# Performance work log

Measured on AMD Instinct MI355X. Metric: run time of the kernel, lower is better.

The kernel has to match this reference:

```python
import jax, jax.numpy as jnp
import numpy as np

RES = 1024
NUM_ROOMS = 8
N_AGENTS = 5_000_000


def setup_inputs() -> dict:
    key = jax.random.key(0)
    k1, k2, k3 = jax.random.split(key, 3)
    agent_positions = jax.random.uniform(k1, (N_AGENTS, 2), dtype=jnp.float32)
    room_params = jax.random.uniform(k2, (NUM_ROOMS, 4), dtype=jnp.float32)
    # torch init: params[:, 2:] = params[:, 2:] * 0.1 + 0.05  (room sigmas)
    room_params = room_params.at[:, 2:].set(room_params[:, 2:] * 0.1 + 0.05)
    wall_density = jax.random.uniform(k3, (RES, RES), dtype=jnp.float32)
    return {
        "agent_positions": agent_positions,
        "room_params": room_params,
        "wall_density": wall_density,
    }


def reference(agent_positions, room_params, wall_density):
    res = wall_density.shape[0]
    lin = jnp.linspace(0.0, 1.0, res, dtype=wall_density.dtype)
    x_grid, y_grid = jnp.meshgrid(lin, lin, indexing="ij")  # [res,res]

    # Per-room Gaussian density maps, vectorized over rooms -> [R,res,res]
    cx = room_params[:, 0, None, None]
    cy = room_params[:, 1, None, None]
    sx = room_params[:, 2, None, None]
    sy = room_params[:, 3, None, None]
    spatial_layout = jnp.exp(
        -((x_grid - cx) ** 2 / (2.0 * sx**2) + (y_grid - cy) ** 2 / (2.0 * sy**2))
    )

    # Agent flow histogram via single fused scatter-add
    ix = jnp.clip((agent_positions[:, 0] * res).astype(jnp.int32), 0, res - 1)
    iy = jnp.clip((agent_positions[:, 1] * res).astype(jnp.int32), 0, res - 1)
    flow_field = jnp.zeros((res, res), dtype=wall_density.dtype).at[ix, iy].add(1.0)
    flow_field = flow_field / (flow_field.max() + 1e-6)

    dynamic_layout = spatial_layout * (1.0 - wall_density[None, :, :])
    return (dynamic_layout, flow_field)
```

## Files before the change

kernel.cpp:

```cpp
#include <hip/hip_runtime.h>

#define RES 1024
#define NROOMS 8
#define NBUCKETS 256
#define BINS_PER_BUCKET (4 * RES)
#define CAP 32768
#define SWPB 8
#define NBLK 512
#define F4PT 10
#define STG_MAX (512 * F4PT * 2)

typedef unsigned int u32x4 __attribute__((ext_vector_type(4)));
typedef float        f32x4 __attribute__((ext_vector_type(4)));

__device__ __forceinline__ void dyn_cell(
    const float* __restrict__ room_params,
    const float4* __restrict__ wall,
    float4* __restrict__ dyn, int idx)
{
    int i  = idx >> 8;
    int j0 = (idx & 255) << 2;
    const float inv1023 = 1.0f / 1023.0f;
    float x  = (float)i * inv1023;
    float y0 = (float)(j0 + 0) * inv1023;
    float y1 = (float)(j0 + 1) * inv1023;
    float y2 = (float)(j0 + 2) * inv1023;
    float y3 = (float)(j0 + 3) * inv1023;

    float4 w = wall[idx];
    float omx = 1.0f - w.x;
    float omy = 1.0f - w.y;
    float omz = 1.0f - w.z;
    float omw = 1.0f - w.w;

    const int plane4 = (RES * RES) / 4;
    #pragma unroll
    for (int r = 0; r < NROOMS; ++r) {
        float cx = room_params[4 * r + 0];
        float cy = room_params[4 * r + 1];
        float sx = room_params[4 * r + 2];
        float sy = room_params[4 * r + 3];
        float isx = 1.0f / (2.0f * sx * sx);
        float isy = 1.0f / (2.0f * sy * sy);
        float dx = x - cx;
        float ax = dx * dx * isx;
        float d0 = y0 - cy, d1 = y1 - cy, d2 = y2 - cy, d3 = y3 - cy;
        f32x4 d;
        d.x = __expf(-(ax + d0 * d0 * isy)) * omx;
        d.y = __expf(-(ax + d1 * d1 * isy)) * omy;
        d.z = __expf(-(ax + d2 * d2 * isy)) * omz;
        d.w = __expf(-(ax + d3 * d3 * isy)) * omw;
        __builtin_nontemporal_store(
            d, reinterpret_cast<f32x4*>(&dyn[(size_t)r * plane4 + idx]));
    }
}

__global__ __launch_bounds__(512, 4) void scatter_kernel(
    const float4* __restrict__ pos, int n4, int nagents,
    unsigned short* __restrict__ buf, unsigned int* __restrict__ cursor,
    const float* __restrict__ room_params,
    const float4* __restrict__ wall,
    float4* __restrict__ dyn)
{
    __shared__ unsigned int   cnt[SWPB][NBUCKETS];
    __shared__ unsigned int   pstart[NBUCKETS];
    __shared__ unsigned int   ptotal[NBUCKETS];
    __shared__ unsigned int   gbase[NBUCKETS];
    __shared__ unsigned int   wsum[4];
    __shared__ unsigned short staged[STG_MAX];
    __shared__ unsigned int   codeLDS[2 * F4PT][512];

    int tid  = threadIdx.x;
    int wv   = tid >> 6;
    int lane = tid & 63;

    #pragma unroll
    for (int i = 0; i < (SWPB * NBUCKETS) / 512; ++i)
        ((unsigned int*)cnt)[tid + 512 * i] = 0u;
    __syncthreads();

    int chunk = (n4 + NBLK - 1) / NBLK;
    int start = blockIdx.x * chunk;
    int end   = min(start + chunk, n4);

    #pragma unroll
    for (int k = 0; k < F4PT; ++k) {
        int i4 = start + (k << 9) + tid;
        if (i4 < end) {
            float4 p = pos[i4];
            int ix0 = min(max((int)(p.x * 1024.0f), 0), 1023);
            int iy0 = min(max((int)(p.y * 1024.0f), 0), 1023);
            int ix1 = min(max((int)(p.z * 1024.0f), 0), 1023);
            int iy1 = min(max((int)(p.w * 1024.0f), 0), 1023);
            unsigned int b0 = (unsigned int)(ix0 >> 2);
            unsigned int b1 = (unsigned int)(ix1 >> 2);
            unsigned int bin0 = (unsigned int)(((ix0 & 3) << 10) | iy0);
            unsigned int bin1 = (unsigned int)(((ix1 & 3) << 10) | iy1);
            unsigned int r0 = atomicAdd(&cnt[wv][b0], 1u);
            unsigned int r1 = atomicAdd(&cnt[wv][b1], 1u);
            codeLDS[2 * k][tid]     = (b0 << 23) | (r0 << 12) | bin0;
            codeLDS[2 * k + 1][tid] = (b1 << 23) | (r1 << 12) | bin1;
        } else {
            codeLDS[2 * k][tid]     = 0xFFFFFFFFu;
            codeLDS[2 * k + 1][tid] = 0xFFFFFFFFu;
        }
    }

    dyn_cell(room_params, wall, dyn, blockIdx.x * 512 + tid);

    __syncthreads();

    if (tid < NBUCKETS) {
        unsigned int run = 0;
        #pragma unroll
        for (int w = 0; w < SWPB; ++w) {
            unsigned int c = cnt[w][tid];
            cnt[w][tid] = run;
            run += c;
        }
        ptotal[tid] = run;
        gbase[tid]  = run ? atomicAdd(&cursor[tid], run) : 0u;
        unsigned int t = run;
        #pragma unroll
        for (int off = 1; off < 64; off <<= 1) {
            unsigned int v = (unsigned int)__shfl_up((int)t, off, 64);
            if (lane >= off) t += v;
        }
        if (lane == 63) wsum[wv] = t;
        pstart[tid] = t - run;
    }
    __syncthreads();
    if (tid < NBUCKETS) {
        unsigned int off = 0;
        #pragma unroll
        for (int w = 0; w < 3; ++w) if (w < wv) off += wsum[w];
        unsigned int ps = pstart[tid] + off;
        pstart[tid] = ps;
        #pragma unroll
        for (int w = 0; w < SWPB; ++w) cnt[w][tid] += ps;
    }
    __syncthreads();

    #pragma unroll
    for (int k = 0; k < 2 * F4PT; ++k) {
        unsigned int u = codeLDS[k][tid];
        if (u != 0xFFFFFFFFu) {
            unsigned int b   = u >> 23;
            unsigned int r   = (u >> 12) & 0x7FFu;
            unsigned int bin = u & 0xFFFu;
            staged[cnt[wv][b] + r] = (unsigned short)bin;
        }
    }
    __syncthreads();

    #pragma unroll 4
    for (int bb = 0; bb < 32; ++bb) {
        int b = (wv << 5) + bb;
        unsigned int n  = ptotal[b];
        unsigned int ps = pstart[b];
        unsigned int gb = gbase[b];
        for (unsigned int e = lane; e < n; e += 64) {
            unsigned int p = gb + e;
            if (p < CAP) buf[b * CAP + p] = staged[ps + e];
        }
    }

    if (blockIdx.x == 0 && tid == 0 && (nagents & 1)) {
        const float* t = (const float*)pos;
        float px = t[2 * (nagents - 1)];
        float py = t[2 * (nagents - 1) + 1];
        int ix = min(max((int)(px * 1024.0f), 0), 1023);
        int iy = min(max((int)(py * 1024.0f), 0), 1023);
        unsigned int b = (unsigned int)(ix >> 2);
        unsigned int p = atomicAdd(&cursor[b], 1u);
        if (p < CAP) buf[b * CAP + p] = (unsigned short)(((ix & 3) << 10) | iy);
    }
}

__global__ __launch_bounds__(1024) void hist_build_kernel(
    const unsigned short* __restrict__ buf,
    const unsigned int* __restrict__ cursor,
    unsigned int* __restrict__ counts,
    unsigned int* __restrict__ out_max)
{
    __shared__ __align__(16) unsigned int h[BINS_PER_BUCKET];
    int b = blockIdx.x, tid = threadIdx.x;
    #pragma unroll
    for (int i = 0; i < BINS_PER_BUCKET / 1024; ++i) h[tid + 1024 * i] = 0u;
    __syncthreads();

    unsigned int n = min(cursor[b], (unsigned int)CAP);
    const unsigned short* seg = buf + (size_t)b * CAP;
    unsigned int n2 = n & ~1u;
    for (unsigned int i = 2 * tid; i < n2; i += 2048) {
        unsigned int u = *(const unsigned int*)(seg + i);
        atomicAdd(&h[u & 0xFFFFu], 1u);
        atomicAdd(&h[u >> 16], 1u);
    }
    if (tid == 0 && (n & 1)) atomicAdd(&h[seg[n - 1]], 1u);
    __syncthreads();

    u32x4 v = ((const u32x4*)h)[tid];
    ((u32x4*)counts)[(size_t)b * (BINS_PER_BUCKET / 4) + tid] = v;
    unsigned int m = max(max(v.x, v.y), max(v.z, v.w));
    #pragma unroll
    for (int off = 32; off > 0; off >>= 1)
        m = max(m, (unsigned int)__shfl_down((int)m, off, 64));
    __shared__ unsigned int sm[16];
    if ((tid & 63) == 0) sm[tid >> 6] = m;
    __syncthreads();
    if (tid == 0) {
        #pragma unroll
        for (int w = 1; w < 16; ++w) m = max(m, sm[w]);
        atomicMax(out_max, m);
    }
}

__global__ __launch_bounds__(256) void norm_kernel(
    float* __restrict__ flow, const unsigned int* __restrict__ maxp)
{
    int idx = blockIdx.x * blockDim.x + threadIdx.x;
    uint4 c = ((const uint4*)flow)[idx];
    float inv = 1.0f / ((float)(*maxp) + 1e-6f);
    ((float4*)flow)[idx] = make_float4((float)c.x * inv, (float)c.y * inv,
                                       (float)c.z * inv, (float)c.w * inv);
}

__global__ __launch_bounds__(256) void hist_atomic_kernel(
    const float4* __restrict__ pos, int n4, int nagents,
    unsigned int* __restrict__ counts)
{
    int idx = blockIdx.x * blockDim.x + threadIdx.x;
    int stride = gridDim.x * blockDim.x;
    for (int i = idx; i < n4; i += stride) {
        float4 p = pos[i];
        int ix0 = min(max((int)(p.x * 1024.0f), 0), 1023);
        int iy0 = min(max((int)(p.y * 1024.0f), 0), 1023);
        int ix1 = min(max((int)(p.z * 1024.0f), 0), 1023);
        int iy1 = min(max((int)(p.w * 1024.0f), 0), 1023);
        atomicAdd(&counts[(ix0 << 10) + iy0], 1u);
        atomicAdd(&counts[(ix1 << 10) + iy1], 1u);
    }
    if (idx == 0 && (nagents & 1)) {
        const float* t = (const float*)pos;
        int ix = min(max((int)(t[2 * (nagents - 1)] * 1024.0f), 0), 1023);
        int iy = min(max((int)(t[2 * (nagents - 1) + 1] * 1024.0f), 0), 1023);
        atomicAdd(&counts[(ix << 10) + iy], 1u);
    }
}

__global__ __launch_bounds__(256) void max_kernel(
    const uint4* __restrict__ counts, unsigned int* __restrict__ out_max)
{
    int idx = blockIdx.x * blockDim.x + threadIdx.x;
    int stride = gridDim.x * blockDim.x;
    unsigned int m = 0;
    const int n4 = (RES * RES) / 4;
    for (int i = idx; i < n4; i += stride) {
        uint4 c = counts[i];
        m = max(m, max(max(c.x, c.y), max(c.z, c.w)));
    }
    #pragma unroll
    for (int off = 32; off > 0; off >>= 1)
        m = max(m, (unsigned int)__shfl_down((int)m, off, 64));
    __shared__ unsigned int sm[4];
    if ((threadIdx.x & 63) == 0) sm[threadIdx.x >> 6] = m;
    __syncthreads();
    if (threadIdx.x == 0) {
        m = max(max(sm[0], sm[1]), max(sm[2], sm[3]));
        atomicMax(out_max, m);
    }
}

__global__ __launch_bounds__(256) void final_full_kernel(
    const float* __restrict__ room_params,
    const float4* __restrict__ wall,
    float4* __restrict__ dyn,
    float* __restrict__ flow,
    const unsigned int* __restrict__ maxp)
{
    int idx = blockIdx.x * blockDim.x + threadIdx.x;
    uint4 c = ((const uint4*)flow)[idx];
    float inv = 1.0f / ((float)(*maxp) + 1e-6f);
    ((float4*)flow)[idx] = make_float4((float)c.x * inv, (float)c.y * inv,
                                       (float)c.z * inv, (float)c.w * inv);
    dyn_cell(room_params, wall, dyn, idx);
}

extern "C" void kernel_launch(void* const* d_in, const int* in_sizes, int n_in,
                              void* d_out, int out_size, void* d_ws, size_t ws_size,
                              hipStream_t stream) {
    const float* agents      = (const float*)d_in[0];
    const float* room_params = (const float*)d_in[1];
    const float* wall        = (const float*)d_in[2];

    float* dyn  = (float*)d_out;
    float* flow = (float*)d_out + (size_t)NROOMS * RES * RES;
    unsigned int* counts = (unsigned int*)flow;

    int nagents = in_sizes[0] / 2;
    int n4 = nagents / 2;

    size_t need = 2048 + (size_t)NBUCKETS * CAP * sizeof(unsigned short);

    bool fits = ((n4 + NBLK - 1) / NBLK) <= (F4PT * 512);

    if (ws_size >= need && fits) {
        unsigned int*   cursor = (unsigned int*)d_ws;
        unsigned int*   maxp   = (unsigned int*)((char*)d_ws + 1024);
        unsigned short* buf    = (unsigned short*)((char*)d_ws + 2048);

        (void)hipMemsetAsync(d_ws, 0, 2048, stream);
        scatter_kernel<<<NBLK, 512, 0, stream>>>(
            (const float4*)agents, n4, nagents, buf, cursor,
            room_params, (const float4*)wall, (float4*)dyn);
        hist_build_kernel<<<NBUCKETS, 1024, 0, stream>>>(buf, cursor, counts, maxp);
        norm_kernel<<<(RES * RES / 4) / 256, 256, 0, stream>>>(flow, maxp);
    } else {
        unsigned int* maxp = (unsigned int*)d_ws;
        (void)hipMemsetAsync(flow, 0, (size_t)RES * RES * sizeof(float), stream);
        (void)hipMemsetAsync(maxp, 0, sizeof(unsigned int), stream);
        hist_atomic_kernel<<<1280, 256, 0, stream>>>((const float4*)agents, n4, nagents, counts);
        max_kernel<<<256, 256, 0, stream>>>((const uint4*)counts, maxp);
        final_full_kernel<<<(RES * RES / 4) / 256, 256, 0, stream>>>(
            room_params, (const float4*)wall, (float4*)dyn, flow, maxp);
    }
}
```

Before: 118.4 us.

## Fuse normalization into histogram kernel via grid barrier, move dyn work, two-pass scatter

The dynamic-layout computation moves from the scatter kernel into the histogram kernel. The separate normalization kernel is removed: the histogram kernel counts finished blocks with an atomic, spins until all 256 have published their max, then writes normalized floats directly. The scatter kernel now reads positions twice (a count pass, then a placement pass) instead of holding codes in LDS. It also uses 1024 smaller blocks with higher occupancy. This drops one kernel launch and the count round trip through memory, at the cost of re-reading the input and relying on all 256 blocks being co-resident for the spin barrier.

Result: slower. 139.1 us (+17.5%).

```diff
diff --git a/kernel.cpp b/kernel.cpp
--- a/kernel.cpp
+++ b/kernel.cpp
@@ -6,8 +6,8 @@
 #define BINS_PER_BUCKET (4 * RES)
 #define CAP 32768
 #define SWPB 8
-#define NBLK 512
-#define F4PT 10
+#define NBLK 1024
+#define F4PT 5
 #define STG_MAX (512 * F4PT * 2)
 
 typedef unsigned int u32x4 __attribute__((ext_vector_type(4)));
@@ -55,12 +55,9 @@
     }
 }
 
-__global__ __launch_bounds__(512, 4) void scatter_kernel(
+__global__ __launch_bounds__(512, 8) void scatter_kernel(
     const float4* __restrict__ pos, int n4, int nagents,
-    unsigned short* __restrict__ buf, unsigned int* __restrict__ cursor,
-    const float* __restrict__ room_params,
-    const float4* __restrict__ wall,
-    float4* __restrict__ dyn)
+    unsigned short* __restrict__ buf, unsigned int* __restrict__ cursor)
 {
     __shared__ unsigned int   cnt[SWPB][NBUCKETS];
     __shared__ unsigned int   pstart[NBUCKETS];
@@ -68,7 +65,6 @@
     __shared__ unsigned int   gbase[NBUCKETS];
     __shared__ unsigned int   wsum[4];
     __shared__ unsigned short staged[STG_MAX];
-    __shared__ unsigned int   codeLDS[2 * F4PT][512];
 
     int tid  = threadIdx.x;
     int wv   = tid >> 6;
@@ -82,6 +78,50 @@
     int chunk = (n4 + NBLK - 1) / NBLK;
     int start = blockIdx.x * chunk;
     int end   = min(start + chunk, n4);
+
+    #pragma unroll
+    for (int k = 0; k < F4PT; ++k) {
+        int i4 = start + (k << 9) + tid;
+        if (i4 < end) {
+            float4 p = pos[i4];
+            int ix0 = min(max((int)(p.x * 1024.0f), 0), 1023);
+            int ix1 = min(max((int)(p.z * 1024.0f), 0), 1023);
+            atomicAdd(&cnt[wv][ix0 >> 2], 1u);
+            atomicAdd(&cnt[wv][ix1 >> 2], 1u);
+        }
+    }
+    __syncthreads();
+
+    if (tid < NBUCKETS) {
+        unsigned int run = 0;
+        #pragma unroll
+        for (int w = 0; w < SWPB; ++w) {
+            unsigned int c = cnt[w][tid];
+            cnt[w][tid] = run;
+            run += c;
+        }
+        ptotal[tid] = run;
+        gbase[tid]  = run ? atomicAdd(&cursor[tid], run) : 0u;
+        unsigned int t = run;
+        #pragma unroll
+        for (int off = 1; off < 64; off <<= 1) {
+            unsigned int v = (unsigned int)__shfl_up((int)t, off, 64);
+            if (lane >= off) t += v;
+        }
+        if (lane == 63) wsum[wv] = t;
+        pstart[tid] = t - run;
+    }
+    __syncthreads();
+    if (tid < NBUCKETS) {
+        unsigned int off = 0;
+        #pragma unroll
+        for (int w = 0; w < 3; ++w) if (w < wv) off += wsum[w];
+        unsigned int ps = pstart[tid] + off;
+        pstart[tid] = ps;
+        #pragma unroll
+        for (int w = 0; w < SWPB; ++w) cnt[w][tid] += ps;
+    }
+    __syncthreads();
 
     #pragma unroll
     for (int k = 0; k < F4PT; ++k) {
@@ -92,63 +132,10 @@
             int iy0 = min(max((int)(p.y * 1024.0f), 0), 1023);
             int ix1 = min(max((int)(p.z * 1024.0f), 0), 1023);
             int iy1 = min(max((int)(p.w * 1024.0f), 0), 1023);
-            unsigned int b0 = (unsigned int)(ix0 >> 2);
-            unsigned int b1 = (unsigned int)(ix1 >> 2);
-            unsigned int bin0 = (unsigned int)(((ix0 & 3) << 10) | iy0);
-            unsigned int bin1 = (unsigned int)(((ix1 & 3) << 10) | iy1);
-            unsigned int r0 = atomicAdd(&cnt[wv][b0], 1u);
-            unsigned int r1 = atomicAdd(&cnt[wv][b1], 1u);
-            codeLDS[2 * k][tid]     = (b0 << 23) | (r0 << 12) | bin0;
-            codeLDS[2 * k + 1][tid] = (b1 << 23) | (r1 << 12) | bin1;
-        } else {
-            codeLDS[2 * k][tid]     = 0xFFFFFFFFu;
-            codeLDS[2 * k + 1][tid] = 0xFFFFFFFFu;
-        }
-    }
-
-    dyn_cell(room_params, wall, dyn, blockIdx.x * 512 + tid);
-
-    __syncthreads();
-
-    if (tid < NBUCKETS) {
-        unsigned int run = 0;
-        #pragma unroll
-        for (int w = 0; w < SWPB; ++w) {
-            unsigned int c = cnt[w][tid];
-            cnt[w][tid] = run;
-            run += c;
-        }
-        ptotal[tid] = run;
-        gbase[tid]  = run ? atomicAdd(&cursor[tid], run) : 0u;
-        unsigned int t = run;
-        #pragma unroll
-        for (int off = 1; off < 64; off <<= 1) {
-            unsigned int v = (unsigned int)__shfl_up((int)t, off, 64);
-            if (lane >= off) t += v;
-        }
-        if (lane == 63) wsum[wv] = t;
-        pstart[tid] = t - run;
-    }
-    __syncthreads();
-    if (tid < NBUCKETS) {
-        unsigned int off = 0;
-        #pragma unroll
-        for (int w = 0; w < 3; ++w) if (w < wv) off += wsum[w];
-        unsigned int ps = pstart[tid] + off;
-        pstart[tid] = ps;
-        #pragma unroll
-        for (int w = 0; w < SWPB; ++w) cnt[w][tid] += ps;
-    }
-    __syncthreads();
-
-    #pragma unroll
-    for (int k = 0; k < 2 * F4PT; ++k) {
-        unsigned int u = codeLDS[k][tid];
-        if (u != 0xFFFFFFFFu) {
-            unsigned int b   = u >> 23;
-            unsigned int r   = (u >> 12) & 0x7FFu;
-            unsigned int bin = u & 0xFFFu;
-            staged[cnt[wv][b] + r] = (unsigned short)bin;
+            unsigned int s0 = atomicAdd(&cnt[wv][ix0 >> 2], 1u);
+            staged[s0] = (unsigned short)(((ix0 & 3) << 10) | iy0);
+            unsigned int s1 = atomicAdd(&cnt[wv][ix1 >> 2], 1u);
+            staged[s1] = (unsigned short)(((ix1 & 3) << 10) | iy1);
         }
     }
     __syncthreads();
@@ -177,13 +164,19 @@
     }
 }
 
-__global__ __launch_bounds__(1024) void hist_build_kernel(
+__global__ __launch_bounds__(1024) void hist_dyn_kernel(
     const unsigned short* __restrict__ buf,
     const unsigned int* __restrict__ cursor,
-    unsigned int* __restrict__ counts,
-    unsigned int* __restrict__ out_max)
+    const float* __restrict__ room_params,
+    const float4* __restrict__ wall,
+    float4* __restrict__ dyn,
+    float* __restrict__ flow,
+    unsigned int* __restrict__ maxp,
+    unsigned int* __restrict__ done)
 {
     __shared__ __align__(16) unsigned int h[BINS_PER_BUCKET];
+    __shared__ unsigned int sm[16];
+    __shared__ float sinv;
     int b = blockIdx.x, tid = threadIdx.x;
     #pragma unroll
     for (int i = 0; i < BINS_PER_BUCKET / 1024; ++i) h[tid + 1024 * i] = 0u;
@@ -201,29 +194,39 @@
     __syncthreads();
 
     u32x4 v = ((const u32x4*)h)[tid];
-    ((u32x4*)counts)[(size_t)b * (BINS_PER_BUCKET / 4) + tid] = v;
     unsigned int m = max(max(v.x, v.y), max(v.z, v.w));
     #pragma unroll
     for (int off = 32; off > 0; off >>= 1)
         m = max(m, (unsigned int)__shfl_down((int)m, off, 64));
-    __shared__ unsigned int sm[16];
     if ((tid & 63) == 0) sm[tid >> 6] = m;
     __syncthreads();
     if (tid == 0) {
         #pragma unroll
         for (int w = 1; w < 16; ++w) m = max(m, sm[w]);
-        atomicMax(out_max, m);
-    }
-}
-
-__global__ __launch_bounds__(256) void norm_kernel(
-    float* __restrict__ flow, const unsigned int* __restrict__ maxp)
-{
-    int idx = blockIdx.x * blockDim.x + threadIdx.x;
-    uint4 c = ((const uint4*)flow)[idx];
-    float inv = 1.0f / ((float)(*maxp) + 1e-6f);
-    ((float4*)flow)[idx] = make_float4((float)c.x * inv, (float)c.y * inv,
-                                       (float)c.z * inv, (float)c.w * inv);
+        atomicMax(maxp, m);
+        __hip_atomic_fetch_add(done, 1u, __ATOMIC_RELEASE,
+                               __HIP_MEMORY_SCOPE_AGENT);
+    }
+
+    dyn_cell(room_params, wall, dyn, b * 1024 + tid);
+
+    if (tid == 0) {
+        while (__hip_atomic_load(done, __ATOMIC_ACQUIRE,
+                                 __HIP_MEMORY_SCOPE_AGENT) < NBUCKETS)
+            __builtin_amdgcn_s_sleep(8);
+        unsigned int mx = __hip_atomic_load(maxp, __ATOMIC_RELAXED,
+                                            __HIP_MEMORY_SCOPE_AGENT);
+        sinv = 1.0f / ((float)mx + 1e-6f);
+    }
+    __syncthreads();
+    float inv = sinv;
+    f32x4 o;
+    o.x = (float)v.x * inv;
+    o.y = (float)v.y * inv;
+    o.z = (float)v.z * inv;
+    o.w = (float)v.w * inv;
+    __builtin_nontemporal_store(
+        o, reinterpret_cast<f32x4*>(&((float4*)flow)[b * 1024 + tid]));
 }
 
 __global__ __launch_bounds__(256) void hist_atomic_kernel(
@@ -308,14 +311,15 @@
     if (ws_size >= need && fits) {
         unsigned int*   cursor = (unsigned int*)d_ws;
         unsigned int*   maxp   = (unsigned int*)((char*)d_ws + 1024);
+        unsigned int*   done   = (unsigned int*)((char*)d_ws + 1028);
         unsigned short* buf    = (unsigned short*)((char*)d_ws + 2048);
 
         (void)hipMemsetAsync(d_ws, 0, 2048, stream);
         scatter_kernel<<<NBLK, 512, 0, stream>>>(
-            (const float4*)agents, n4, nagents, buf, cursor,
-            room_params, (const float4*)wall, (float4*)dyn);
-        hist_build_kernel<<<NBUCKETS, 1024, 0, stream>>>(buf, cursor, counts, maxp);
-        norm_kernel<<<(RES * RES / 4) / 256, 256, 0, stream>>>(flow, maxp);
+            (const float4*)agents, n4, nagents, buf, cursor);
+        hist_dyn_kernel<<<NBUCKETS, 1024, 0, stream>>>(
+            buf, cursor, room_params, (const float4*)wall, (float4*)dyn,
+            flow, maxp, done);
     } else {
         unsigned int* maxp = (unsigned int*)d_ws;
         (void)hipMemsetAsync(flow, 0, (size_t)RES * RES * sizeof(float), stream);
```

## Drop global bucket cursors and fuse histogram build with normalization via grid barrier

Applied to the files above, without the earlier changes.

The scatter kernel no longer claims global per-bucket slots with atomics. Each block writes its locally sorted staging buffer contiguously and records per-bucket offsets in a meta array, which also removes the memset. The histogram kernel reads each block's segment for its bucket using two threads per source block. It then waits on a spin barrier for the global max and writes normalized floats directly, which removes the separate norm kernel and the counts round trip. In exchange, the barrier assumes all 256 blocks are co-resident, the histogram reads are serial 2-byte loads, and the LDS atomics are less parallel.

New measurement: 167.8 us. +41.8%, slower.

```diff
diff --git a/kernel.cpp b/kernel.cpp
--- a/kernel.cpp
+++ b/kernel.cpp
@@ -4,7 +4,6 @@
 #define NROOMS 8
 #define NBUCKETS 256
 #define BINS_PER_BUCKET (4 * RES)
-#define CAP 32768
 #define SWPB 8
 #define NBLK 512
 #define F4PT 10
@@ -57,22 +56,24 @@
 
 __global__ __launch_bounds__(512, 4) void scatter_kernel(
     const float4* __restrict__ pos, int n4, int nagents,
-    unsigned short* __restrict__ buf, unsigned int* __restrict__ cursor,
+    unsigned short* __restrict__ buf, unsigned short* __restrict__ meta,
+    unsigned int* __restrict__ maxp, unsigned int* __restrict__ done,
     const float* __restrict__ room_params,
     const float4* __restrict__ wall,
     float4* __restrict__ dyn)
 {
     __shared__ unsigned int   cnt[SWPB][NBUCKETS];
     __shared__ unsigned int   pstart[NBUCKETS];
-    __shared__ unsigned int   ptotal[NBUCKETS];
-    __shared__ unsigned int   gbase[NBUCKETS];
     __shared__ unsigned int   wsum[4];
     __shared__ unsigned short staged[STG_MAX];
     __shared__ unsigned int   codeLDS[2 * F4PT][512];
+    __shared__ unsigned int   tailcode;
 
     int tid  = threadIdx.x;
     int wv   = tid >> 6;
     int lane = tid & 63;
+
+    if (blockIdx.x == 0 && tid == 0) { *maxp = 0u; *done = 0u; }
 
     #pragma unroll
     for (int i = 0; i < (SWPB * NBUCKETS) / 512; ++i)
@@ -106,65 +107,6 @@
         }
     }
 
-    dyn_cell(room_params, wall, dyn, blockIdx.x * 512 + tid);
-
-    __syncthreads();
-
-    if (tid < NBUCKETS) {
-        unsigned int run = 0;
-        #pragma unroll
-        for (int w = 0; w < SWPB; ++w) {
-            unsigned int c = cnt[w][tid];
-            cnt[w][tid] = run;
-            run += c;
-        }
-        ptotal[tid] = run;
-        gbase[tid]  = run ? atomicAdd(&cursor[tid], run) : 0u;
-        unsigned int t = run;
-        #pragma unroll
-        for (int off = 1; off < 64; off <<= 1) {
-            unsigned int v = (unsigned int)__shfl_up((int)t, off, 64);
-            if (lane >= off) t += v;
-        }
-        if (lane == 63) wsum[wv] = t;
-        pstart[tid] = t - run;
-    }
-    __syncthreads();
-    if (tid < NBUCKETS) {
-        unsigned int off = 0;
-        #pragma unroll
-        for (int w = 0; w < 3; ++w) if (w < wv) off += wsum[w];
-        unsigned int ps = pstart[tid] + off;
-        pstart[tid] = ps;
-        #pragma unroll
-        for (int w = 0; w < SWPB; ++w) cnt[w][tid] += ps;
-    }
-    __syncthreads();
-
-    #pragma unroll
-    for (int k = 0; k < 2 * F4PT; ++k) {
-        unsigned int u = codeLDS[k][tid];
-        if (u != 0xFFFFFFFFu) {
-            unsigned int b   = u >> 23;
-            unsigned int r   = (u >> 12) & 0x7FFu;
-            unsigned int bin = u & 0xFFFu;
-            staged[cnt[wv][b] + r] = (unsigned short)bin;
-        }
-    }
-    __syncthreads();
-
-    #pragma unroll 4
-    for (int bb = 0; bb < 32; ++bb) {
-        int b = (wv << 5) + bb;
-        unsigned int n  = ptotal[b];
-        unsigned int ps = pstart[b];
-        unsigned int gb = gbase[b];
-        for (unsigned int e = lane; e < n; e += 64) {
-            unsigned int p = gb + e;
-            if (p < CAP) buf[b * CAP + p] = staged[ps + e];
-        }
-    }
-
     if (blockIdx.x == 0 && tid == 0 && (nagents & 1)) {
         const float* t = (const float*)pos;
         float px = t[2 * (nagents - 1)];
@@ -172,58 +114,133 @@
         int ix = min(max((int)(px * 1024.0f), 0), 1023);
         int iy = min(max((int)(py * 1024.0f), 0), 1023);
         unsigned int b = (unsigned int)(ix >> 2);
-        unsigned int p = atomicAdd(&cursor[b], 1u);
-        if (p < CAP) buf[b * CAP + p] = (unsigned short)(((ix & 3) << 10) | iy);
-    }
-}
-
-__global__ __launch_bounds__(1024) void hist_build_kernel(
+        unsigned int r = atomicAdd(&cnt[0][b], 1u);
+        tailcode = (b << 23) | (r << 12)
+                 | (unsigned int)(((ix & 3) << 10) | iy);
+    }
+
+    dyn_cell(room_params, wall, dyn, blockIdx.x * 512 + tid);
+
+    __syncthreads();
+
+    if (tid < NBUCKETS) {
+        unsigned int run = 0;
+        #pragma unroll
+        for (int w = 0; w < SWPB; ++w) {
+            unsigned int c = cnt[w][tid];
+            cnt[w][tid] = run;
+            run += c;
+        }
+        unsigned int t = run;
+        #pragma unroll
+        for (int off = 1; off < 64; off <<= 1) {
+            unsigned int v = (unsigned int)__shfl_up((int)t, off, 64);
+            if (lane >= off) t += v;
+        }
+        if (lane == 63) wsum[wv] = t;
+        pstart[tid] = t - run;
+    }
+    __syncthreads();
+    if (tid < NBUCKETS) {
+        unsigned int off = 0;
+        #pragma unroll
+        for (int w = 0; w < 3; ++w) if (w < wv) off += wsum[w];
+        unsigned int ps = pstart[tid] + off;
+        pstart[tid] = ps;
+        #pragma unroll
+        for (int w = 0; w < SWPB; ++w) cnt[w][tid] += ps;
+        meta[blockIdx.x * NBUCKETS + tid] = (unsigned short)ps;
+    }
+    __syncthreads();
+
+    #pragma unroll
+    for (int k = 0; k < 2 * F4PT; ++k) {
+        unsigned int u = codeLDS[k][tid];
+        if (u != 0xFFFFFFFFu) {
+            unsigned int b   = u >> 23;
+            unsigned int r   = (u >> 12) & 0x7FFu;
+            staged[cnt[wv][b] + r] = (unsigned short)(u & 0xFFFu);
+        }
+    }
+    if (blockIdx.x == 0 && tid == 0 && (nagents & 1)) {
+        unsigned int u = tailcode;
+        staged[cnt[0][u >> 23] + ((u >> 12) & 0x7FFu)]
+            = (unsigned short)(u & 0xFFFu);
+    }
+    __syncthreads();
+
+    unsigned int tot = 2u * (unsigned int)(end - start)
+                     + ((blockIdx.x == 0 && (nagents & 1)) ? 1u : 0u);
+    unsigned int nw = (tot + 1u) >> 1;
+    unsigned int* dst = (unsigned int*)(buf + (size_t)blockIdx.x * STG_MAX);
+    const unsigned int* src = (const unsigned int*)staged;
+    for (unsigned int i = tid; i < nw; i += 512) dst[i] = src[i];
+}
+
+__global__ __launch_bounds__(1024) void hist_norm_kernel(
     const unsigned short* __restrict__ buf,
-    const unsigned int* __restrict__ cursor,
-    unsigned int* __restrict__ counts,
-    unsigned int* __restrict__ out_max)
+    const unsigned short* __restrict__ meta,
+    int n4, int nagents,
+    float* __restrict__ flow,
+    unsigned int* __restrict__ maxp,
+    unsigned int* __restrict__ done)
 {
     __shared__ __align__(16) unsigned int h[BINS_PER_BUCKET];
+    __shared__ unsigned int sm[16];
+    __shared__ float sinv;
     int b = blockIdx.x, tid = threadIdx.x;
     #pragma unroll
     for (int i = 0; i < BINS_PER_BUCKET / 1024; ++i) h[tid + 1024 * i] = 0u;
     __syncthreads();
 
-    unsigned int n = min(cursor[b], (unsigned int)CAP);
-    const unsigned short* seg = buf + (size_t)b * CAP;
-    unsigned int n2 = n & ~1u;
-    for (unsigned int i = 2 * tid; i < n2; i += 2048) {
-        unsigned int u = *(const unsigned int*)(seg + i);
-        atomicAdd(&h[u & 0xFFFFu], 1u);
-        atomicAdd(&h[u >> 16], 1u);
-    }
-    if (tid == 0 && (n & 1)) atomicAdd(&h[seg[n - 1]], 1u);
+    int B    = tid >> 1;
+    int half = tid & 1;
+    int chunk = (n4 + NBLK - 1) / NBLK;
+    int start = B * chunk;
+    int end   = min(start + chunk, n4);
+    unsigned int tot = 2u * (unsigned int)(end - start)
+                     + ((B == 0 && (nagents & 1)) ? 1u : 0u);
+    unsigned int s = meta[B * NBUCKETS + b];
+    unsigned int e = (b < NBUCKETS - 1) ? (unsigned int)meta[B * NBUCKETS + b + 1]
+                                        : tot;
+    unsigned int c  = e - s;
+    unsigned int c0 = (c + 1u) >> 1;
+    unsigned int lo = s + (half ? c0 : 0u);
+    unsigned int hi = half ? e : (s + c0);
+    const unsigned short* seg = buf + (size_t)B * STG_MAX;
+    for (unsigned int i = lo; i < hi; ++i)
+        atomicAdd(&h[seg[i]], 1u);
     __syncthreads();
 
     u32x4 v = ((const u32x4*)h)[tid];
-    ((u32x4*)counts)[(size_t)b * (BINS_PER_BUCKET / 4) + tid] = v;
     unsigned int m = max(max(v.x, v.y), max(v.z, v.w));
     #pragma unroll
     for (int off = 32; off > 0; off >>= 1)
         m = max(m, (unsigned int)__shfl_down((int)m, off, 64));
-    __shared__ unsigned int sm[16];
     if ((tid & 63) == 0) sm[tid >> 6] = m;
     __syncthreads();
     if (tid == 0) {
         #pragma unroll
         for (int w = 1; w < 16; ++w) m = max(m, sm[w]);
-        atomicMax(out_max, m);
-    }
-}
-
-__global__ __launch_bounds__(256) void norm_kernel(
-    float* __restrict__ flow, const unsigned int* __restrict__ maxp)
-{
-    int idx = blockIdx.x * blockDim.x + threadIdx.x;
-    uint4 c = ((const uint4*)flow)[idx];
-    float inv = 1.0f / ((float)(*maxp) + 1e-6f);
-    ((float4*)flow)[idx] = make_float4((float)c.x * inv, (float)c.y * inv,
-                                       (float)c.z * inv, (float)c.w * inv);
+        atomicMax(maxp, m);
+        __hip_atomic_fetch_add(done, 1u, __ATOMIC_RELEASE,
+                               __HIP_MEMORY_SCOPE_AGENT);
+        while (__hip_atomic_load(done, __ATOMIC_ACQUIRE,
+                                 __HIP_MEMORY_SCOPE_AGENT) < NBUCKETS)
+            __builtin_amdgcn_s_sleep(8);
+        unsigned int mx = __hip_atomic_load(maxp, __ATOMIC_RELAXED,
+                                            __HIP_MEMORY_SCOPE_AGENT);
+        sinv = 1.0f / ((float)mx + 1e-6f);
+    }
+    __syncthreads();
+    float inv = sinv;
+    f32x4 o;
+    o.x = (float)v.x * inv;
+    o.y = (float)v.y * inv;
+    o.z = (float)v.z * inv;
+    o.w = (float)v.w * inv;
+    __builtin_nontemporal_store(
+        o, reinterpret_cast<f32x4*>(&((float4*)flow)[b * 1024 + tid]));
 }
 
 __global__ __launch_bounds__(256) void hist_atomic_kernel(
@@ -301,21 +318,23 @@
     int nagents = in_sizes[0] / 2;
     int n4 = nagents / 2;
 
-    size_t need = 2048 + (size_t)NBUCKETS * CAP * sizeof(unsigned short);
+    size_t meta_off = 1024;
+    size_t buf_off  = 512 * 1024;
+    size_t need = buf_off + (size_t)NBLK * STG_MAX * sizeof(unsigned short);
 
     bool fits = ((n4 + NBLK - 1) / NBLK) <= (F4PT * 512);
 
     if (ws_size >= need && fits) {
-        unsigned int*   cursor = (unsigned int*)d_ws;
-        unsigned int*   maxp   = (unsigned int*)((char*)d_ws + 1024);
-        unsigned short* buf    = (unsigned short*)((char*)d_ws + 2048);
-
-        (void)hipMemsetAsync(d_ws, 0, 2048, stream);
+        unsigned int*   maxp = (unsigned int*)d_ws;
+        unsigned int*   done = (unsigned int*)((char*)d_ws + 4);
+        unsigned short* meta = (unsigned short*)((char*)d_ws + meta_off);
+        unsigned short* buf  = (unsigned short*)((char*)d_ws + buf_off);
+
         scatter_kernel<<<NBLK, 512, 0, stream>>>(
-            (const float4*)agents, n4, nagents, buf, cursor,
+            (const float4*)agents, n4, nagents, buf, meta, maxp, done,
             room_params, (const float4*)wall, (float4*)dyn);
-        hist_build_kernel<<<NBUCKETS, 1024, 0, stream>>>(buf, cursor, counts, maxp);
-        norm_kernel<<<(RES * RES / 4) / 256, 256, 0, stream>>>(flow, maxp);
+        hist_norm_kernel<<<NBUCKETS, 1024, 0, stream>>>(
+            buf, meta, n4, nagents, flow, maxp, done);
     } else {
         unsigned int* maxp = (unsigned int*)d_ws;
         (void)hipMemsetAsync(flow, 0, (size_t)RES * RES * sizeof(float), stream);
```

## Fuse histogram build and normalization via grid-wide atomic barrier

Applied to the files above, without the earlier changes.

Merges the histogram build and normalization kernels into one. Each block publishes its bucket max, signals a global done counter, and spins until all 256 blocks arrive. It then normalizes its own bins from registers and writes floats with nontemporal stores. This removes a kernel launch and the write-then-reread of the 4 MB count array, but it depends on all 256 blocks of 1024 threads being co-resident, or the spin barrier deadlocks.

After: 127.6 us. 1.08x slower.

```diff
diff --git a/kernel.cpp b/kernel.cpp
--- a/kernel.cpp
+++ b/kernel.cpp
@@ -177,13 +177,16 @@
     }
 }
 
-__global__ __launch_bounds__(1024) void hist_build_kernel(
+__global__ __launch_bounds__(1024) void hist_norm_kernel(
     const unsigned short* __restrict__ buf,
     const unsigned int* __restrict__ cursor,
-    unsigned int* __restrict__ counts,
-    unsigned int* __restrict__ out_max)
+    float* __restrict__ flow,
+    unsigned int* __restrict__ maxp,
+    unsigned int* __restrict__ done)
 {
     __shared__ __align__(16) unsigned int h[BINS_PER_BUCKET];
+    __shared__ unsigned int sm[16];
+    __shared__ float sinv;
     int b = blockIdx.x, tid = threadIdx.x;
     #pragma unroll
     for (int i = 0; i < BINS_PER_BUCKET / 1024; ++i) h[tid + 1024 * i] = 0u;
@@ -201,29 +204,34 @@
     __syncthreads();
 
     u32x4 v = ((const u32x4*)h)[tid];
-    ((u32x4*)counts)[(size_t)b * (BINS_PER_BUCKET / 4) + tid] = v;
     unsigned int m = max(max(v.x, v.y), max(v.z, v.w));
     #pragma unroll
     for (int off = 32; off > 0; off >>= 1)
         m = max(m, (unsigned int)__shfl_down((int)m, off, 64));
-    __shared__ unsigned int sm[16];
     if ((tid & 63) == 0) sm[tid >> 6] = m;
     __syncthreads();
     if (tid == 0) {
         #pragma unroll
         for (int w = 1; w < 16; ++w) m = max(m, sm[w]);
-        atomicMax(out_max, m);
-    }
-}
-
-__global__ __launch_bounds__(256) void norm_kernel(
-    float* __restrict__ flow, const unsigned int* __restrict__ maxp)
-{
-    int idx = blockIdx.x * blockDim.x + threadIdx.x;
-    uint4 c = ((const uint4*)flow)[idx];
-    float inv = 1.0f / ((float)(*maxp) + 1e-6f);
-    ((float4*)flow)[idx] = make_float4((float)c.x * inv, (float)c.y * inv,
-                                       (float)c.z * inv, (float)c.w * inv);
+        atomicMax(maxp, m);
+        __hip_atomic_fetch_add(done, 1u, __ATOMIC_RELEASE,
+                               __HIP_MEMORY_SCOPE_AGENT);
+        while (__hip_atomic_load(done, __ATOMIC_ACQUIRE,
+                                 __HIP_MEMORY_SCOPE_AGENT) < NBUCKETS)
+            __builtin_amdgcn_s_sleep(8);
+        unsigned int mx = __hip_atomic_load(maxp, __ATOMIC_RELAXED,
+                                            __HIP_MEMORY_SCOPE_AGENT);
+        sinv = 1.0f / ((float)mx + 1e-6f);
+    }
+    __syncthreads();
+    float inv = sinv;
+    f32x4 o;
+    o.x = (float)v.x * inv;
+    o.y = (float)v.y * inv;
+    o.z = (float)v.z * inv;
+    o.w = (float)v.w * inv;
+    __builtin_nontemporal_store(
+        o, reinterpret_cast<f32x4*>(&((float4*)flow)[b * 1024 + tid]));
 }
 
 __global__ __launch_bounds__(256) void hist_atomic_kernel(
@@ -308,14 +316,15 @@
     if (ws_size >= need && fits) {
         unsigned int*   cursor = (unsigned int*)d_ws;
         unsigned int*   maxp   = (unsigned int*)((char*)d_ws + 1024);
+        unsigned int*   done   = (unsigned int*)((char*)d_ws + 1028);
         unsigned short* buf    = (unsigned short*)((char*)d_ws + 2048);
 
         (void)hipMemsetAsync(d_ws, 0, 2048, stream);
         scatter_kernel<<<NBLK, 512, 0, stream>>>(
             (const float4*)agents, n4, nagents, buf, cursor,
             room_params, (const float4*)wall, (float4*)dyn);
-        hist_build_kernel<<<NBUCKETS, 1024, 0, stream>>>(buf, cursor, counts, maxp);
-        norm_kernel<<<(RES * RES / 4) / 256, 256, 0, stream>>>(flow, maxp);
+        hist_norm_kernel<<<NBUCKETS, 1024, 0, stream>>>(
+            buf, cursor, flow, maxp, done);
     } else {
         unsigned int* maxp = (unsigned int*)d_ws;
         (void)hipMemsetAsync(flow, 0, (size_t)RES * RES * sizeof(float), stream);
```
